# Performance work log

Measured on AMD Instinct MI355X. Metric: run time of the kernel, lower is better.

The kernel has to match this reference:

```python
import jax, jax.numpy as jnp
import numpy as np

P_ERR = 0.1  # channel error probability (init arg error_prob)


def setup_inputs() -> dict:
    key = jax.random.key(0)
    k1, k2, k3 = jax.random.split(key, 3)
    B, L, V = 1024, 32, 1024
    messages = jax.random.uniform(k1, (B, L, V), dtype=jnp.float32)
    probs = jax.random.uniform(k2, (B, L, V), dtype=jnp.float32)
    # mask over non-EOS columns, torch.rand(...) < p with the module's generator
    target_mask = jax.random.bernoulli(k3, P_ERR, (B * L, V - 1))
    return {"messages": messages, "probs": probs, "target_mask": target_mask}


def reference(messages, probs, target_mask):
    # SymmetricChannel.forward in training mode:
    # returns (process(noise=True), process(noise=False)), flattened to 4 arrays.
    B, L, V = messages.shape
    flat = messages.reshape(B * L, V)
    m = target_mask.astype(flat.dtype)                 # [BL, V-1]
    T = flat[:, 1:] * m                                 # target symbol values at masked cols
    inv = 1.0 / (V - 2)
    # each masked target t at col c adds t/(V-2) to every non-EOS col of its row
    # and -t at col c itself (replacing the t/(V-2) contribution there)
    row_sum = jnp.sum(T, axis=-1, keepdims=True)        # [BL, 1]
    delta = row_sum * inv - T * (1.0 + inv)             # [BL, V-1]
    noisy_flat_tail = flat[:, 1:] + delta
    noisy_messages = jnp.concatenate([flat[:, :1], noisy_flat_tail], axis=-1).reshape(B, L, V)
    # probability adjustment: symbol kept w.p. (1-p), replaced uniformly over V-2 others
    p_rep = (1.0 - probs[..., 1:] - probs[..., :1]) * (P_ERR * inv)
    noisy_tail = probs[..., 1:] * (1.0 - P_ERR) + p_rep
    noisy_probs = jnp.concatenate([probs[..., :1], noisy_tail], axis=-1)
    # (noisy messages, noisy probs, clean messages, clean probs)
    return (noisy_messages, noisy_probs, messages, probs)
```

## Files before the change

### kernel.cpp

```cpp
#include <hip/hip_runtime.h>


constexpr int V   = 1024;
constexpr int VM1 = V - 1;

__global__ __launch_bounds__(256)
void symchan_kernel(const float* __restrict__ msgs,
                    const float* __restrict__ probs,
                    const int*   __restrict__ mask,
                    float*       __restrict__ out,
                    long long N)
{
    const int r = blockIdx.x;
    const int t = threadIdx.x;
    const long long rowBase = (long long)r * V;
    const long long idx = rowBase + 4LL * t;

    const float4 mv = *reinterpret_cast<const float4*>(msgs  + idx);
    const float4 pv = *reinterpret_cast<const float4*>(probs + idx);

    const int* mk = mask + (long long)r * VM1;
    const int j0 = t << 2;
    const float m0 = (t == 0) ? 0.0f : (mk[j0 - 1] ? 1.0f : 0.0f);
    const float m1 = mk[j0 + 0] ? 1.0f : 0.0f;
    const float m2 = mk[j0 + 1] ? 1.0f : 0.0f;
    const float m3 = mk[j0 + 2] ? 1.0f : 0.0f;

    const float T0 = mv.x * m0;
    const float T1 = mv.y * m1;
    const float T2 = mv.z * m2;
    const float T3 = mv.w * m3;

    float partial = (T0 + T1) + (T2 + T3);
    #pragma unroll
    for (int off = 32; off > 0; off >>= 1)
        partial += __shfl_down(partial, off, 64);

    __shared__ float wsum[4];
    __shared__ float p0s;
    const int lane = t & 63;
    const int wid  = t >> 6;
    if (lane == 0) wsum[wid] = partial;
    if (t == 0)    p0s = pv.x;
    __syncthreads();
    const float row_sum = (wsum[0] + wsum[1]) + (wsum[2] + wsum[3]);
    const float p0 = p0s;

    constexpr float inv = 1.0f / (float)(V - 2);
    constexpr float P   = 0.1f;
    const float add = row_sum * inv;
    const float c1  = 1.0f + inv;

    float4 nm;
    nm.x = (t == 0) ? mv.x : mv.x + add - T0 * c1;
    nm.y = mv.y + add - T1 * c1;
    nm.z = mv.z + add - T2 * c1;
    nm.w = mv.w + add - T3 * c1;

    const float q  = 1.0f - P;
    const float pc = P * inv;
    float4 npv;
    npv.x = (t == 0) ? pv.x : pv.x * q + (1.0f - pv.x - p0) * pc;
    npv.y = pv.y * q + (1.0f - pv.y - p0) * pc;
    npv.z = pv.z * q + (1.0f - pv.z - p0) * pc;
    npv.w = pv.w * q + (1.0f - pv.w - p0) * pc;

    *reinterpret_cast<float4*>(out + idx)            = nm;
    *reinterpret_cast<float4*>(out + N + idx)        = npv;
    *reinterpret_cast<float4*>(out + 2 * N + idx)    = mv;
    *reinterpret_cast<float4*>(out + 3 * N + idx)    = pv;
}

extern "C" void kernel_launch(void* const* d_in, const int* in_sizes, int n_in,
                              void* d_out, int out_size, void* d_ws, size_t ws_size,
                              hipStream_t stream) {
    const float* msgs  = (const float*)d_in[0];
    const float* probs = (const float*)d_in[1];
    const int*   mask  = (const int*)d_in[2];
    float* out = (float*)d_out;

    const long long N  = (long long)in_sizes[0];
    const int       BL = (int)(N / V);

    symchan_kernel<<<BL, 256, 0, stream>>>(msgs, probs, mask, out, N);
}
```

Baseline: 179.9 us.

## Map one row per wavefront with shuffle reduction and nontemporal memory ops

Each 64-lane wavefront now handles a whole row, with four float4 chunks per lane. The row sum is done by an xor-shuffle butterfly, which removes the shared-memory reduction and the block barrier. Loads and stores use nontemporal builtins to avoid polluting the cache on this streaming kernel, and the grid shrinks by four. Each thread now holds more registers, and the mask reads become strided per lane.

```diff
diff --git a/kernel.cpp b/kernel.cpp
--- a/kernel.cpp
+++ b/kernel.cpp
@@ -3,6 +3,8 @@
 
 constexpr int V   = 1024;
 constexpr int VM1 = V - 1;
+
+typedef float f4 __attribute__((ext_vector_type(4)));
 
 __global__ __launch_bounds__(256)
 void symchan_kernel(const float* __restrict__ msgs,
@@ -11,64 +13,79 @@
                     float*       __restrict__ out,
                     long long N)
 {
-    const int r = blockIdx.x;
-    const int t = threadIdx.x;
-    const long long rowBase = (long long)r * V;
-    const long long idx = rowBase + 4LL * t;
+    const int wid  = threadIdx.x >> 6;
+    const int lane = threadIdx.x & 63;
+    const long long row = (long long)blockIdx.x * 4 + wid;
+    const long long rowBase = row * V;
+    const int* mk = mask + row * (long long)VM1;
 
-    const float4 mv = *reinterpret_cast<const float4*>(msgs  + idx);
-    const float4 pv = *reinterpret_cast<const float4*>(probs + idx);
+    f4 mv[4], pv[4];
+    float T[4][4];
 
-    const int* mk = mask + (long long)r * VM1;
-    const int j0 = t << 2;
-    const float m0 = (t == 0) ? 0.0f : (mk[j0 - 1] ? 1.0f : 0.0f);
-    const float m1 = mk[j0 + 0] ? 1.0f : 0.0f;
-    const float m2 = mk[j0 + 1] ? 1.0f : 0.0f;
-    const float m3 = mk[j0 + 2] ? 1.0f : 0.0f;
+    #pragma unroll
+    for (int c = 0; c < 4; ++c) {
+        const int j0 = 256 * c + 4 * lane;
+        mv[c] = __builtin_nontemporal_load(
+                    reinterpret_cast<const f4*>(msgs + rowBase + j0));
+        pv[c] = __builtin_nontemporal_load(
+                    reinterpret_cast<const f4*>(probs + rowBase + j0));
+    }
 
-    const float T0 = mv.x * m0;
-    const float T1 = mv.y * m1;
-    const float T2 = mv.z * m2;
-    const float T3 = mv.w * m3;
+    #pragma unroll
+    for (int c = 0; c < 4; ++c) {
+        const int j0 = 256 * c + 4 * lane;
+        const float m0 = (j0 == 0) ? 0.0f : (mk[j0 - 1] ? 1.0f : 0.0f);
+        const float m1 = mk[j0 + 0] ? 1.0f : 0.0f;
+        const float m2 = mk[j0 + 1] ? 1.0f : 0.0f;
+        const float m3 = mk[j0 + 2] ? 1.0f : 0.0f;
+        T[c][0] = mv[c].x * m0;
+        T[c][1] = mv[c].y * m1;
+        T[c][2] = mv[c].z * m2;
+        T[c][3] = mv[c].w * m3;
+    }
 
-    float partial = (T0 + T1) + (T2 + T3);
+    float partial = 0.0f;
     #pragma unroll
-    for (int off = 32; off > 0; off >>= 1)
-        partial += __shfl_down(partial, off, 64);
+    for (int c = 0; c < 4; ++c)
+        partial += (T[c][0] + T[c][1]) + (T[c][2] + T[c][3]);
 
-    __shared__ float wsum[4];
-    __shared__ float p0s;
-    const int lane = t & 63;
-    const int wid  = t >> 6;
-    if (lane == 0) wsum[wid] = partial;
-    if (t == 0)    p0s = pv.x;
-    __syncthreads();
-    const float row_sum = (wsum[0] + wsum[1]) + (wsum[2] + wsum[3]);
-    const float p0 = p0s;
+    #pragma unroll
+    for (int m = 1; m < 64; m <<= 1)
+        partial += __shfl_xor(partial, m, 64);
+    const float row_sum = partial;
+
+    const float p0 = __shfl(pv[0].x, 0, 64);
 
     constexpr float inv = 1.0f / (float)(V - 2);
     constexpr float P   = 0.1f;
     const float add = row_sum * inv;
     const float c1  = 1.0f + inv;
+    const float q   = 1.0f - P;
+    const float pc  = P * inv;
 
-    float4 nm;
-    nm.x = (t == 0) ? mv.x : mv.x + add - T0 * c1;
-    nm.y = mv.y + add - T1 * c1;
-    nm.z = mv.z + add - T2 * c1;
-    nm.w = mv.w + add - T3 * c1;
+    #pragma unroll
+    for (int c = 0; c < 4; ++c) {
+        const int j0 = 256 * c + 4 * lane;
+        const long long idx = rowBase + j0;
+        const bool col0 = (j0 == 0);
 
-    const float q  = 1.0f - P;
-    const float pc = P * inv;
-    float4 npv;
-    npv.x = (t == 0) ? pv.x : pv.x * q + (1.0f - pv.x - p0) * pc;
-    npv.y = pv.y * q + (1.0f - pv.y - p0) * pc;
-    npv.z = pv.z * q + (1.0f - pv.z - p0) * pc;
-    npv.w = pv.w * q + (1.0f - pv.w - p0) * pc;
+        f4 nm;
+        nm.x = col0 ? mv[c].x : mv[c].x + add - T[c][0] * c1;
+        nm.y = mv[c].y + add - T[c][1] * c1;
+        nm.z = mv[c].z + add - T[c][2] * c1;
+        nm.w = mv[c].w + add - T[c][3] * c1;
 
-    *reinterpret_cast<float4*>(out + idx)            = nm;
-    *reinterpret_cast<float4*>(out + N + idx)        = npv;
-    *reinterpret_cast<float4*>(out + 2 * N + idx)    = mv;
-    *reinterpret_cast<float4*>(out + 3 * N + idx)    = pv;
+        f4 np;
+        np.x = col0 ? pv[c].x : pv[c].x * q + (1.0f - pv[c].x - p0) * pc;
+        np.y = pv[c].y * q + (1.0f - pv[c].y - p0) * pc;
+        np.z = pv[c].z * q + (1.0f - pv[c].z - p0) * pc;
+        np.w = pv[c].w * q + (1.0f - pv[c].w - p0) * pc;
+
+        __builtin_nontemporal_store(nm,    reinterpret_cast<f4*>(out + idx));
+        __builtin_nontemporal_store(np,    reinterpret_cast<f4*>(out + N + idx));
+        __builtin_nontemporal_store(mv[c], reinterpret_cast<f4*>(out + 2 * N + idx));
+        __builtin_nontemporal_store(pv[c], reinterpret_cast<f4*>(out + 3 * N + idx));
+    }
 }
 
 extern "C" void kernel_launch(void* const* d_in, const int* in_sizes, int n_in,
@@ -81,6 +98,7 @@
 
     const long long N  = (long long)in_sizes[0];
     const int       BL = (int)(N / V);
+    const int       nb = BL / 4;
 
-    symchan_kernel<<<BL, 256, 0, stream>>>(msgs, probs, mask, out, N);
+    symchan_kernel<<<nb, 256, 0, stream>>>(msgs, probs, mask, out, N);
 }
```

Result: faster. 149.7 us (-16.8%).
